# Performance work log

Hardware: AMD Instinct MI355X
Metric: run time of the kernel (lower is better)

Reference implementation:

```python
import jax, jax.numpy as jnp
import numpy as np

N = 50000        # total nodes across batch
K = 16           # max neighbors per node (padded with index 0)
E = 800000       # directed edges / messages
B = 1024         # molecules
MAXM = 48        # max nodes per molecule (padded with index 0)
FEATURE_FDIM = 9
ALL_FDIM = 10    # feature_dist_graph (9) + reshaped rij distance (1)
H = 64           # hidden_dim
NUM_ITERS = 2
NEG_INF = -1e9


def setup_inputs() -> dict:
    key = jax.random.key(0)
    ks = jax.random.split(key, 16)
    s = 1.0 / np.sqrt(H)
    return {
        "target_features": jax.random.normal(ks[0], (N, FEATURE_FDIM), jnp.float32),
        "feature_dist_graph": jax.random.normal(ks[1], (E, ALL_FDIM - 1), jnp.float32),
        "rij_dist_pairs": jax.random.uniform(ks[2], (E,), jnp.float32),
        "start_end_env": jax.random.randint(ks[3], (N, K), 0, N + 1),
        "b_scope": jax.random.randint(ks[4], (N, K), 0, E),
        "l_scope": jax.random.randint(ks[5], (B, MAXM), 0, N + 1),
        "scope_update": jax.random.randint(ks[6], (E,), 0, N + 1),
        "scope_update_lig": jax.random.randint(ks[7], (E,), 0, N + 1),
        "W_emb": jax.random.uniform(ks[8], (FEATURE_FDIM, H), jnp.float32, 0.1, 0.9),
        "b_emb": jnp.zeros((H,), jnp.float32),
        "W_dist": jax.random.uniform(ks[9], (ALL_FDIM, H), jnp.float32, 0.1, 0.9),
        "b_dist": jnp.zeros((H,), jnp.float32),
        "W_gat": jax.random.normal(ks[10], (H, H), jnp.float32) * s,
        "Wm_gat": jax.random.normal(ks[11], (H, H), jnp.float32) * s,
        "a_gat": jax.random.normal(ks[12], (2 * H,), jnp.float32) * s,
    }


def reference(target_features, feature_dist_graph, rij_dist_pairs,
              start_end_env, b_scope, l_scope, scope_update, scope_update_lig,
              W_emb, b_emb, W_dist, b_dist, W_gat, Wm_gat, a_gat):
    # node embedding over origin features
    h = target_features @ W_emb + b_emb                        # [N, H]
    # edge message embedding over pair features + distance
    msg_in = jnp.concatenate([feature_dist_graph, rij_dist_pairs[:, None]], axis=1)
    message = msg_in @ W_dist + b_dist                         # [E, H]
    # prepend zero pad row (index 0 = padding for ragged gathers)
    hp = jnp.concatenate([jnp.zeros((1, H), h.dtype), h], axis=0)  # [N+1, H]
    pad_mask = (start_end_env == 0)                            # [N, K]
    upd_mask = (scope_update_lig > 0).astype(h.dtype)[:, None]  # [E, 1]
    for _ in range(NUM_ITERS):
        nb = hp[start_end_env]                                 # [N, K, H] gather neighbors
        mg = message[b_scope]                                  # [N, K, H] gather messages
        Wn = nb @ W_gat                                        # [N, K, H]
        Wm = mg @ Wm_gat                                       # [N, K, H]
        # GAT attention logits: leaky_relu(a^T [Wn || Wm])
        logits = jax.nn.leaky_relu(
            jnp.einsum('nkh,h->nk', Wn, a_gat[:H]) +
            jnp.einsum('nkh,h->nk', Wm, a_gat[H:]), 0.2)       # [N, K]
        logits = jnp.where(pad_mask, NEG_INF, logits)
        alpha = jax.nn.softmax(logits, axis=1)                 # [N, K]
        new_h = jax.nn.elu(jnp.einsum('nk,nkh->nh', alpha, Wn + Wm))  # [N, H]
        hp = jnp.concatenate([jnp.zeros((1, H), new_h.dtype), new_h], axis=0)
        # scatter updated node features back into edge messages
        message = hp[scope_update] * upd_mask                  # [E, H]
    cmp_enc = hp[l_scope]                                      # [B, MAXM, H]
    return cmp_enc.sum(axis=1)                                 # [B, H]
```

## Files before the change

kernel.cpp:

```cpp
#include <hip/hip_runtime.h>
#include <hip/hip_bf16.h>

#define N_NODES 50000
#define K_NB 16
#define E_EDGES 800000
#define B_MOL 1024
#define MAXM_M 48
#define FDIM 9
#define ADIM 10
#define H 64
#define NEG_INF_F (-1e9f)
#define PRE_NODE_BLOCKS 196
#define EDGE_BLOCKS 3125

typedef __bf16 bf16x8 __attribute__((ext_vector_type(8)));
typedef float f32x4 __attribute__((ext_vector_type(4)));

__device__ inline float readlane_f(float v, int l) {
    return __int_as_float(__builtin_amdgcn_readlane(__float_as_int(v), l));
}
__device__ inline int readlane_i(int v, int l) {
    return __builtin_amdgcn_readlane(v, l);
}
__device__ inline float bf2f(unsigned u) {
    return __uint_as_float(u << 16);
}
__device__ inline unsigned short f2bf(float f) {
    unsigned x = __float_as_uint(f);
    return (unsigned short)((x + 0x7fffu + ((x >> 16) & 1u)) >> 16);
}

#define GLOAD_U16(dst, voff, sbase) \
    asm volatile("global_load_ushort %0, %1, %2" : "=v"(dst) : "v"(voff), "s"(sbase))
#define GLOAD_F32(dst, voff, sbase) \
    asm volatile("global_load_dword %0, %1, %2" : "=v"(dst) : "v"(voff), "s"(sbase))
#define GLOAD_DW(dst, voff, sbase) \
    asm volatile("global_load_dword %0, %1, %2" : "=v"(dst) : "v"(voff), "s"(sbase))

#define DRAIN16(a) \
    asm volatile("s_waitcnt vmcnt(0)" \
        : "+v"(a[0]), "+v"(a[1]), "+v"(a[2]), "+v"(a[3]), \
          "+v"(a[4]), "+v"(a[5]), "+v"(a[6]), "+v"(a[7]), \
          "+v"(a[8]), "+v"(a[9]), "+v"(a[10]), "+v"(a[11]), \
          "+v"(a[12]), "+v"(a[13]), "+v"(a[14]), "+v"(a[15]))
#define HOLD16(a) \
    asm volatile("" \
        : "+v"(a[0]), "+v"(a[1]), "+v"(a[2]), "+v"(a[3]), \
          "+v"(a[4]), "+v"(a[5]), "+v"(a[6]), "+v"(a[7]), \
          "+v"(a[8]), "+v"(a[9]), "+v"(a[10]), "+v"(a[11]), \
          "+v"(a[12]), "+v"(a[13]), "+v"(a[14]), "+v"(a[15]))

__global__ __launch_bounds__(256) void k_fold(
    const float* __restrict__ W_emb, const float* __restrict__ b_emb,
    const float* __restrict__ W_dist, const float* __restrict__ b_dist,
    const float* __restrict__ W_gat, const float* __restrict__ Wm_gat,
    const float* __restrict__ a_gat,
    float* __restrict__ W2, float* __restrict__ c2,
    float* __restrict__ W3, float* __restrict__ c3,
    float* __restrict__ wa, float* __restrict__ ca,
    float* __restrict__ va, float* __restrict__ vb,
    float* __restrict__ wv9, float* __restrict__ cv,
    unsigned short* __restrict__ WintT)
{
    __shared__ float s_va[64], s_vb[64];
    int tid = threadIdx.x;
    int h = tid & 63, g = tid >> 6;
    if (g == 0) {
        float acc = 0.f;
        for (int t = 0; t < H; ++t) acc += W_gat[h * H + t] * a_gat[t];
        s_va[h] = acc; va[h] = acc;
    } else if (g == 1) {
        float acc = 0.f;
        for (int t = 0; t < H; ++t) acc += Wm_gat[h * H + t] * a_gat[H + t];
        s_vb[h] = acc; vb[h] = acc;
    } else if (g == 2) {
        float acc = 0.f;
        for (int t = 0; t < H; ++t) acc += b_dist[t] * Wm_gat[t * H + h];
        c2[h] = acc;
    } else {
        float acc = 0.f;
        for (int t = 0; t < H; ++t) acc += b_emb[t] * W_gat[t * H + h];
        c3[h] = acc;
    }
    __syncthreads();
    for (int q = tid; q < 640; q += 256) {
        int j = q >> 6, hh = q & 63;
        float acc = 0.f;
        for (int t = 0; t < H; ++t) acc += W_dist[j * H + t] * Wm_gat[t * H + hh];
        W2[q] = acc;
    }
    for (int q = tid; q < 576; q += 256) {
        int j = q >> 6, hh = q & 63;
        float acc = 0.f;
        for (int t = 0; t < H; ++t) acc += W_emb[j * H + t] * W_gat[t * H + hh];
        W3[q] = acc;
    }
    for (int q = tid; q < H * 2 * H; q += 256) {
        int n = q >> 7, k = q & 127;
        float v = (k & 1) ? Wm_gat[(k >> 1) * H + n] : W_gat[(k >> 1) * H + n];
        WintT[q] = f2bf(v);
    }
    if (tid < ADIM) {
        float acc = 0.f;
        for (int t = 0; t < H; ++t) acc += W_dist[tid * H + t] * s_vb[t];
        wa[tid] = acc;
    } else if (tid == ADIM) {
        float acc = 0.f;
        for (int t = 0; t < H; ++t) acc += b_dist[t] * s_vb[t];
        ca[0] = acc;
    } else if (tid >= 16 && tid < 16 + FDIM) {
        int j = tid - 16;
        float acc = 0.f;
        for (int t = 0; t < H; ++t) acc += W_emb[j * H + t] * s_va[t];
        wv9[j] = acc;
    } else if (tid == 31) {
        float acc = 0.f;
        for (int t = 0; t < H; ++t) acc += b_emb[t] * s_va[t];
        cv[0] = acc;
    }
}

__global__ __launch_bounds__(256) void k_pre(
    const float* __restrict__ tf, const float* __restrict__ fdg,
    const float* __restrict__ rij,
    const int* __restrict__ su, const int* __restrict__ sul,
    const float* __restrict__ wa, const float* __restrict__ ca,
    const float* __restrict__ wv9, const float* __restrict__ cv,
    float* __restrict__ t1A, unsigned short* __restrict__ tfp,
    unsigned short* __restrict__ emsg, int* __restrict__ sue)
{
    int bid = blockIdx.x;
    if (bid < PRE_NODE_BLOCKS) {
        int n = bid * 256 + threadIdx.x;
        if (n == 0) {
            t1A[0] = 0.f;
            uint4 z = make_uint4(0, 0, 0, 0);
            ((uint4*)tfp)[0] = z; ((uint4*)tfp)[1] = z;
        }
        if (n >= N_NODES) return;
        float f[FDIM];
        float acc = cv[0];
#pragma unroll
        for (int j = 0; j < FDIM; ++j) {
            f[j] = tf[n * FDIM + j];
            acc += f[j] * wv9[j];
        }
        t1A[n + 1] = acc;
        unsigned rec[8];
#pragma unroll
        for (int j = 0; j < 4; ++j)
            rec[j] = (unsigned)f2bf(f[2 * j]) | ((unsigned)f2bf(f[2 * j + 1]) << 16);
        rec[4] = (unsigned)f2bf(f[8]);
        rec[5] = 0; rec[6] = 0; rec[7] = 0;
        uint4* dst = (uint4*)(tfp + (size_t)(n + 1) * 16);
        dst[0] = make_uint4(rec[0], rec[1], rec[2], rec[3]);
        dst[1] = make_uint4(rec[4], rec[5], rec[6], rec[7]);
    } else {
        int e = (bid - PRE_NODE_BLOCKS) * 256 + threadIdx.x;
        float f[ADIM];
#pragma unroll
        for (int j = 0; j < FDIM; ++j) f[j] = fdg[(size_t)e * FDIM + j];
        f[FDIM] = rij[e];
        float acc = ca[0];
#pragma unroll
        for (int j = 0; j < ADIM; ++j) acc += f[j] * wa[j];
        unsigned rec[8];
#pragma unroll
        for (int j = 0; j < 5; ++j)
            rec[j] = (unsigned)f2bf(f[2 * j]) | ((unsigned)f2bf(f[2 * j + 1]) << 16);
        rec[5] = __float_as_uint(acc);
        rec[6] = 0; rec[7] = 0;
        uint4* dst = (uint4*)(emsg + (size_t)e * 16);
        dst[0] = make_uint4(rec[0], rec[1], rec[2], rec[3]);
        dst[1] = make_uint4(rec[4], rec[5], rec[6], rec[7]);
        sue[e] = (sul[e] > 0) ? su[e] : 0;
    }
}

__global__ __launch_bounds__(256) void k_gat1(
    const int* __restrict__ sse, const int* __restrict__ bsc,
    const float* __restrict__ t1A, const unsigned short* __restrict__ tfp,
    const unsigned short* __restrict__ emsg,
    const float* __restrict__ W2, const float* __restrict__ c2,
    const float* __restrict__ W3, const float* __restrict__ c3,
    const float* __restrict__ va, const float* __restrict__ vb,
    unsigned short* __restrict__ hp2bf, float* __restrict__ t1B,
    float* __restrict__ t2B)
{
    int wave = threadIdx.x >> 6;
    int lane = threadIdx.x & 63;
    int n = blockIdx.x * 4 + wave;
    if (n == 0) {
        hp2bf[lane] = 0;
        if (lane == 0) { t1B[0] = 0.f; t2B[0] = 0.f; }
    }
    if (n >= N_NODES) return;

    int kidx = 0, ke = 0;
    float lg = NEG_INF_F;
    if (lane < K_NB) {
        kidx = sse[n * K_NB + lane];
        ke   = bsc[n * K_NB + lane];
        float g2 = __uint_as_float(*(const unsigned*)(emsg + (size_t)ke * 16 + 10));
        float p = t1A[kidx] + g2;
        p = (p > 0.f) ? p : 0.2f * p;
        lg = (kidx == 0) ? NEG_INF_F : p;
    }

    unsigned wn_u[K_NB], wm_u[K_NB];
    int offr = (lane & 15) * 2;
#pragma unroll
    for (int k = 0; k < K_NB; ++k) {
        const unsigned short* pk = tfp + (size_t)readlane_i(kidx, k) * 16;
        GLOAD_U16(wn_u[k], offr, pk);
    }
#pragma unroll
    for (int k = 0; k < K_NB; ++k) {
        const unsigned short* pe = emsg + (size_t)readlane_i(ke, k) * 16;
        GLOAD_U16(wm_u[k], offr, pe);
    }

    float m = lg;
#pragma unroll
    for (int o = 8; o > 0; o >>= 1) m = fmaxf(m, __shfl_xor(m, o, 64));
    float ex = __expf(lg - m);
    float s = ex;
#pragma unroll
    for (int o = 8; o > 0; o >>= 1) s += __shfl_xor(s, o, 64);
    float alpha = ex / s;

    DRAIN16(wn_u);
    HOLD16(wm_u);

    float fr = 0.f, frm = 0.f, beta = 0.f;
#pragma unroll
    for (int k = 0; k < K_NB; ++k) {
        float ak = readlane_f(alpha, k);
        fr  += ak * bf2f(wn_u[k]);
        frm += ak * bf2f(wm_u[k]);
        beta += (readlane_i(kidx, k) > 0) ? ak : 0.f;
    }
    float acc = c2[lane] + beta * c3[lane];
#pragma unroll
    for (int j = 0; j < FDIM; ++j) acc += readlane_f(fr, j) * W3[j * H + lane];
#pragma unroll
    for (int j = 0; j < ADIM; ++j) acc += readlane_f(frm, j) * W2[j * H + lane];
    float o = (acc > 0.f) ? acc : expm1f(acc);
    hp2bf[(size_t)(n + 1) * H + lane] = f2bf(o);
    float ta = o * va[lane], tb = o * vb[lane];
#pragma unroll
    for (int q = 32; q > 0; q >>= 1) {
        ta += __shfl_xor(ta, q, 64);
        tb += __shfl_xor(tb, q, 64);
    }
    if (lane == 0) { t1B[n + 1] = ta; t2B[n + 1] = tb; }
}

__global__ __launch_bounds__(1024) void k_gat2(
    const int* __restrict__ sse, const int* __restrict__ bsc,
    const int* __restrict__ sue,
    const float* __restrict__ t1B, const float* __restrict__ t2B,
    const unsigned short* __restrict__ hp2bf,
    const unsigned short* __restrict__ WintT,
    float* __restrict__ hp3)
{
    __shared__ unsigned s_rows[16][72];
    int wave = threadIdx.x >> 6;
    int lane = threadIdx.x & 63;
    int row  = blockIdx.x * 16 + wave;
    int n    = row - 1;

    float gn0 = 0.f, gn1 = 0.f, gm0 = 0.f, gm1 = 0.f;
    if (n >= 0 && n < N_NODES) {
        int kidx = 0, ksu = 0;
        float lg = NEG_INF_F;
        if (lane < K_NB) {
            kidx = sse[n * K_NB + lane];
            int ke = bsc[n * K_NB + lane];
            ksu = sue[ke];
            float p = t1B[kidx] + t2B[ksu];
            p = (p > 0.f) ? p : 0.2f * p;
            lg = (kidx == 0) ? NEG_INF_F : p;
        }

        int halfsel = lane >> 5;
        int cbyte = (lane & 31) * 4;
        unsigned wp[16];
#pragma unroll
        for (int g = 0; g < 8; ++g) {
            int rA = readlane_i(kidx, g);
            int rB = readlane_i(kidx, g + 8);
            int r  = halfsel ? rB : rA;
            GLOAD_DW(wp[g], r * 128 + cbyte, hp2bf);
        }
#pragma unroll
        for (int g = 0; g < 8; ++g) {
            int sA = readlane_i(ksu, g);
            int sB = readlane_i(ksu, g + 8);
            int rs = halfsel ? sB : sA;
            GLOAD_DW(wp[8 + g], rs * 128 + cbyte, hp2bf);
        }

        float m = lg;
#pragma unroll
        for (int o = 8; o > 0; o >>= 1) m = fmaxf(m, __shfl_xor(m, o, 64));
        float ex = __expf(lg - m);
        float s = ex;
#pragma unroll
        for (int o = 8; o > 0; o >>= 1) s += __shfl_xor(s, o, 64);
        float alpha = ex / s;

        DRAIN16(wp);

#pragma unroll
        for (int g = 0; g < 8; ++g) {
            float aA = readlane_f(alpha, g);
            float aB = readlane_f(alpha, g + 8);
            float av = halfsel ? aB : aA;
            unsigned wn = wp[g], wm = wp[8 + g];
            gn0 += av * bf2f(wn & 0xffffu);
            gn1 += av * bf2f(wn >> 16);
            gm0 += av * bf2f(wm & 0xffffu);
            gm1 += av * bf2f(wm >> 16);
        }
        gn0 += __shfl_xor(gn0, 32, 64);
        gn1 += __shfl_xor(gn1, 32, 64);
        gm0 += __shfl_xor(gm0, 32, 64);
        gm1 += __shfl_xor(gm1, 32, 64);
    }
    if (lane < 32) {
        s_rows[wave][2 * lane]     = (unsigned)f2bf(gn0) | ((unsigned)f2bf(gm0) << 16);
        s_rows[wave][2 * lane + 1] = (unsigned)f2bf(gn1) | ((unsigned)f2bf(gm1) << 16);
    }
    __syncthreads();

    if (wave < 4) {
        int t = wave;
        int m = lane & 15, q = lane >> 4;
        union UB { uint4 u; bf16x8 v; };
        bf16x8 bfr[4];
        const unsigned short* bp = WintT + (size_t)(t * 16 + m) * 128 + q * 8;
#pragma unroll
        for (int kk = 0; kk < 4; ++kk) {
            UB ub; ub.u = *(const uint4*)(bp + kk * 32);
            bfr[kk] = ub.v;
        }
        f32x4 acc = (f32x4){0.f, 0.f, 0.f, 0.f};
#pragma unroll
        for (int kk = 0; kk < 4; ++kk) {
            UB ua; ua.u = *(const uint4*)&s_rows[m][kk * 16 + q * 4];
            acc = __builtin_amdgcn_mfma_f32_16x16x32_bf16(ua.v, bfr[kk], acc, 0, 0, 0);
        }
        int row0 = blockIdx.x * 16;
#pragma unroll
        for (int r = 0; r < 4; ++r) {
            int rr = row0 + q * 4 + r;
            if (rr <= N_NODES) {
                float v = acc[r];
                hp3[(size_t)rr * H + t * 16 + m] = (v > 0.f) ? v : expm1f(v);
            }
        }
    }
}

__global__ __launch_bounds__(256) void k_out(
    const int* __restrict__ l_scope, const float* __restrict__ hp,
    float* __restrict__ out)
{
    int wave = threadIdx.x >> 6;
    int lane = threadIdx.x & 63;
    int b = blockIdx.x * 4 + wave;
    if (b >= B_MOL) return;
    int idx48 = (lane < MAXM_M) ? l_scope[b * MAXM_M + lane] : 0;
    float v[MAXM_M];
    int off = lane * 4;
#pragma unroll
    for (int m = 0; m < MAXM_M; ++m) {
        const float* pm = hp + (size_t)readlane_i(idx48, m) * H;
        GLOAD_F32(v[m], off, pm);
    }
    asm volatile("s_waitcnt vmcnt(0)"
        : "+v"(v[0]), "+v"(v[1]), "+v"(v[2]), "+v"(v[3]),
          "+v"(v[4]), "+v"(v[5]), "+v"(v[6]), "+v"(v[7]),
          "+v"(v[8]), "+v"(v[9]), "+v"(v[10]), "+v"(v[11]),
          "+v"(v[12]), "+v"(v[13]), "+v"(v[14]), "+v"(v[15]));
    asm volatile(""
        : "+v"(v[16]), "+v"(v[17]), "+v"(v[18]), "+v"(v[19]),
          "+v"(v[20]), "+v"(v[21]), "+v"(v[22]), "+v"(v[23]),
          "+v"(v[24]), "+v"(v[25]), "+v"(v[26]), "+v"(v[27]),
          "+v"(v[28]), "+v"(v[29]), "+v"(v[30]), "+v"(v[31]));
    asm volatile(""
        : "+v"(v[32]), "+v"(v[33]), "+v"(v[34]), "+v"(v[35]),
          "+v"(v[36]), "+v"(v[37]), "+v"(v[38]), "+v"(v[39]),
          "+v"(v[40]), "+v"(v[41]), "+v"(v[42]), "+v"(v[43]),
          "+v"(v[44]), "+v"(v[45]), "+v"(v[46]), "+v"(v[47]));
    float acc = 0.f;
#pragma unroll
    for (int m = 0; m < MAXM_M; ++m) acc += v[m];
    out[b * H + lane] = acc;
}

extern "C" void kernel_launch(void* const* d_in, const int* in_sizes, int n_in,
                              void* d_out, int out_size, void* d_ws, size_t ws_size,
                              hipStream_t stream)
{
    const float* tf     = (const float*)d_in[0];
    const float* fdg    = (const float*)d_in[1];
    const float* rij    = (const float*)d_in[2];
    const int*   sse    = (const int*)d_in[3];
    const int*   bsc    = (const int*)d_in[4];
    const int*   lsc    = (const int*)d_in[5];
    const int*   su     = (const int*)d_in[6];
    const int*   sul    = (const int*)d_in[7];
    const float* W_emb  = (const float*)d_in[8];
    const float* b_emb  = (const float*)d_in[9];
    const float* W_dist = (const float*)d_in[10];
    const float* b_dist = (const float*)d_in[11];
    const float* W_gat  = (const float*)d_in[12];
    const float* Wm_gat = (const float*)d_in[13];
    const float* a_gat  = (const float*)d_in[14];
    float* out = (float*)d_out;

    char* base = (char*)d_ws;
    size_t off = 0;
    auto alloc = [&](size_t bytes) {
        char* p = base + off;
        off = (off + bytes + 255) & ~(size_t)255;
        return p;
    };
    float* W2   = (float*)alloc(640 * 4);
    float* c2   = (float*)alloc(64 * 4);
    float* W3   = (float*)alloc(640 * 4);
    float* c3   = (float*)alloc(64 * 4);
    float* wa   = (float*)alloc(16 * 4);
    float* ca   = (float*)alloc(16 * 4);
    float* va   = (float*)alloc(64 * 4);
    float* vb   = (float*)alloc(64 * 4);
    float* wv9  = (float*)alloc(16 * 4);
    float* cv   = (float*)alloc(16 * 4);
    unsigned short* WintT = (unsigned short*)alloc(64 * 128 * 2);
    float* t1A  = (float*)alloc((size_t)(N_NODES + 1) * 4);
    float* t1B  = (float*)alloc((size_t)(N_NODES + 1) * 4);
    float* t2B  = (float*)alloc((size_t)(N_NODES + 1) * 4);
    int*   sue  = (int*)alloc((size_t)E_EDGES * 4);
    unsigned short* tfp   = (unsigned short*)alloc((size_t)(N_NODES + 1) * 16 * 2);
    unsigned short* hp2bf = (unsigned short*)alloc((size_t)(N_NODES + 1) * H * 2);
    char* big = alloc((size_t)E_EDGES * 32);
    unsigned short* emsg = (unsigned short*)big;
    float* hp3 = (float*)big;

    k_fold<<<dim3(1), dim3(256), 0, stream>>>(
        W_emb, b_emb, W_dist, b_dist, W_gat, Wm_gat, a_gat,
        W2, c2, W3, c3, wa, ca, va, vb, wv9, cv, WintT);

    k_pre<<<dim3(PRE_NODE_BLOCKS + EDGE_BLOCKS), dim3(256), 0, stream>>>(
        tf, fdg, rij, su, sul, wa, ca, wv9, cv, t1A, tfp, emsg, sue);

    k_gat1<<<dim3((N_NODES + 3) / 4), dim3(256), 0, stream>>>(
        sse, bsc, t1A, tfp, emsg, W2, c2, W3, c3, va, vb, hp2bf, t1B, t2B);

    k_gat2<<<dim3((N_NODES + 16) / 16), dim3(1024), 0, stream>>>(
        sse, bsc, sue, t1B, t2B, hp2bf, WintT, hp3);

    k_out<<<dim3(B_MOL / 4), dim3(256), 0, stream>>>(lsc, hp3, out);
}
```

Baseline: 208.2 us.

## Pack gat1 neighbor gathers across lane quarters and halve gat2 block size

In k_gat1, each of the four 16-lane quarters now gathers a different neighbor row, so 4 loads per array replace 16, with lane-partial sums combined by xor shuffles. Beta becomes a wave reduction instead of a serial readlane loop. k_gat2 moves to 512-thread blocks covering 8 rows, zero-pads the unused half of the shared MFMA tile, and only stores the valid rows. This cuts VGPR pressure and load-issue count in gat1 and raises block count in gat2, at the cost of extra shuffles and MFMA work wasted on padding rows.

```diff
diff --git a/kernel.cpp b/kernel.cpp
--- a/kernel.cpp
+++ b/kernel.cpp
@@ -43,12 +43,10 @@
           "+v"(a[4]), "+v"(a[5]), "+v"(a[6]), "+v"(a[7]), \
           "+v"(a[8]), "+v"(a[9]), "+v"(a[10]), "+v"(a[11]), \
           "+v"(a[12]), "+v"(a[13]), "+v"(a[14]), "+v"(a[15]))
-#define HOLD16(a) \
-    asm volatile("" \
+#define DRAIN8(a, b) \
+    asm volatile("s_waitcnt vmcnt(0)" \
         : "+v"(a[0]), "+v"(a[1]), "+v"(a[2]), "+v"(a[3]), \
-          "+v"(a[4]), "+v"(a[5]), "+v"(a[6]), "+v"(a[7]), \
-          "+v"(a[8]), "+v"(a[9]), "+v"(a[10]), "+v"(a[11]), \
-          "+v"(a[12]), "+v"(a[13]), "+v"(a[14]), "+v"(a[15]))
+          "+v"(b[0]), "+v"(b[1]), "+v"(b[2]), "+v"(b[3]))
 
 __global__ __launch_bounds__(256) void k_fold(
     const float* __restrict__ W_emb, const float* __restrict__ b_emb,
@@ -207,17 +205,31 @@
         lg = (kidx == 0) ? NEG_INF_F : p;
     }
 
-    unsigned wn_u[K_NB], wm_u[K_NB];
-    int offr = (lane & 15) * 2;
-#pragma unroll
-    for (int k = 0; k < K_NB; ++k) {
-        const unsigned short* pk = tfp + (size_t)readlane_i(kidx, k) * 16;
-        GLOAD_U16(wn_u[k], offr, pk);
-    }
-#pragma unroll
-    for (int k = 0; k < K_NB; ++k) {
-        const unsigned short* pe = emsg + (size_t)readlane_i(ke, k) * 16;
-        GLOAD_U16(wm_u[k], offr, pe);
+    int q1 = lane & 16;
+    int q2 = lane & 32;
+    int elem2 = (lane & 15) * 2;
+    unsigned wn_u[4], wm_u[4];
+#pragma unroll
+    for (int g = 0; g < 4; ++g) {
+        int rA = readlane_i(kidx, g);
+        int rB = readlane_i(kidx, g + 4);
+        int rC = readlane_i(kidx, g + 8);
+        int rD = readlane_i(kidx, g + 12);
+        int rLo = q1 ? rB : rA;
+        int rHi = q1 ? rD : rC;
+        int r   = q2 ? rHi : rLo;
+        GLOAD_U16(wn_u[g], r * 32 + elem2, tfp);
+    }
+#pragma unroll
+    for (int g = 0; g < 4; ++g) {
+        int rA = readlane_i(ke, g);
+        int rB = readlane_i(ke, g + 4);
+        int rC = readlane_i(ke, g + 8);
+        int rD = readlane_i(ke, g + 12);
+        int rLo = q1 ? rB : rA;
+        int rHi = q1 ? rD : rC;
+        int r   = q2 ? rHi : rLo;
+        GLOAD_U16(wm_u[g], r * 32 + elem2, emsg);
     }
 
     float m = lg;
@@ -229,17 +241,28 @@
     for (int o = 8; o > 0; o >>= 1) s += __shfl_xor(s, o, 64);
     float alpha = ex / s;
 
-    DRAIN16(wn_u);
-    HOLD16(wm_u);
-
-    float fr = 0.f, frm = 0.f, beta = 0.f;
-#pragma unroll
-    for (int k = 0; k < K_NB; ++k) {
-        float ak = readlane_f(alpha, k);
-        fr  += ak * bf2f(wn_u[k]);
-        frm += ak * bf2f(wm_u[k]);
-        beta += (readlane_i(kidx, k) > 0) ? ak : 0.f;
-    }
+    float beta = (kidx > 0) ? alpha : 0.f;
+#pragma unroll
+    for (int o = 1; o <= 32; o <<= 1) beta += __shfl_xor(beta, o, 64);
+
+    DRAIN8(wn_u, wm_u);
+
+    float fr = 0.f, frm = 0.f;
+#pragma unroll
+    for (int g = 0; g < 4; ++g) {
+        float aA = readlane_f(alpha, g);
+        float aB = readlane_f(alpha, g + 4);
+        float aC = readlane_f(alpha, g + 8);
+        float aD = readlane_f(alpha, g + 12);
+        float aLo = q1 ? aB : aA;
+        float aHi = q1 ? aD : aC;
+        float av  = q2 ? aHi : aLo;
+        fr  += av * bf2f(wn_u[g]);
+        frm += av * bf2f(wm_u[g]);
+    }
+    fr  += __shfl_xor(fr, 16, 64);  fr  += __shfl_xor(fr, 32, 64);
+    frm += __shfl_xor(frm, 16, 64); frm += __shfl_xor(frm, 32, 64);
+
     float acc = c2[lane] + beta * c3[lane];
 #pragma unroll
     for (int j = 0; j < FDIM; ++j) acc += readlane_f(fr, j) * W3[j * H + lane];
@@ -256,7 +279,7 @@
     if (lane == 0) { t1B[n + 1] = ta; t2B[n + 1] = tb; }
 }
 
-__global__ __launch_bounds__(1024) void k_gat2(
+__global__ __launch_bounds__(512) void k_gat2(
     const int* __restrict__ sse, const int* __restrict__ bsc,
     const int* __restrict__ sue,
     const float* __restrict__ t1B, const float* __restrict__ t2B,
@@ -267,8 +290,13 @@
     __shared__ unsigned s_rows[16][72];
     int wave = threadIdx.x >> 6;
     int lane = threadIdx.x & 63;
-    int row  = blockIdx.x * 16 + wave;
+    int row  = blockIdx.x * 8 + wave;
     int n    = row - 1;
+
+    if (lane < 32) {
+        s_rows[wave + 8][2 * lane]     = 0u;
+        s_rows[wave + 8][2 * lane + 1] = 0u;
+    }
 
     float gn0 = 0.f, gn1 = 0.f, gm0 = 0.f, gm1 = 0.f;
     if (n >= 0 && n < N_NODES) {
@@ -351,13 +379,15 @@
             UB ua; ua.u = *(const uint4*)&s_rows[m][kk * 16 + q * 4];
             acc = __builtin_amdgcn_mfma_f32_16x16x32_bf16(ua.v, bfr[kk], acc, 0, 0, 0);
         }
-        int row0 = blockIdx.x * 16;
-#pragma unroll
-        for (int r = 0; r < 4; ++r) {
-            int rr = row0 + q * 4 + r;
-            if (rr <= N_NODES) {
-                float v = acc[r];
-                hp3[(size_t)rr * H + t * 16 + m] = (v > 0.f) ? v : expm1f(v);
+        int row0 = blockIdx.x * 8;
+        if (q < 2) {
+#pragma unroll
+            for (int r = 0; r < 4; ++r) {
+                int rr = row0 + q * 4 + r;
+                if (rr <= N_NODES) {
+                    float v = acc[r];
+                    hp3[(size_t)rr * H + t * 16 + m] = (v > 0.f) ? v : expm1f(v);
+                }
             }
         }
     }
@@ -459,7 +489,7 @@
     k_gat1<<<dim3((N_NODES + 3) / 4), dim3(256), 0, stream>>>(
         sse, bsc, t1A, tfp, emsg, W2, c2, W3, c3, va, vb, hp2bf, t1B, t2B);
 
-    k_gat2<<<dim3((N_NODES + 16) / 16), dim3(1024), 0, stream>>>(
+    k_gat2<<<dim3((N_NODES + 8) / 8), dim3(512), 0, stream>>>(
         sse, bsc, sue, t1B, t2B, hp2bf, WintT, hp3);
 
     k_out<<<dim3(B_MOL / 4), dim3(256), 0, stream>>>(lsc, hp3, out);
```

Measured after the change: 202.8 us, median of 2. -2.6%, faster.

## Vectorize gat1 neighbor gathers with dwordx2 loads and shrink gat2 blocks

Applied to the files above, without the earlier changes.

In k_gat1, the 32 serialized per-neighbor ushort gathers are replaced by one dwordx2 gather per lane for node features and one for edge messages. Each group of four lanes covers one neighbor row, with indices broadcast via ds_bpermute, and the weighted sums are reduced with cross-lane shuffles. The separate edge logit load is also folded into the message gather. k_gat2 moves from 1024-thread blocks of 16 rows to 512-thread blocks of 8 rows, zero-padding the unused MFMA rows, which costs half of the MFMA work but gives smaller blocks and finer scheduling.

```diff
diff --git a/kernel.cpp b/kernel.cpp
--- a/kernel.cpp
+++ b/kernel.cpp
@@ -15,6 +15,7 @@
 
 typedef __bf16 bf16x8 __attribute__((ext_vector_type(8)));
 typedef float f32x4 __attribute__((ext_vector_type(4)));
+typedef unsigned u32x2 __attribute__((ext_vector_type(2)));
 
 __device__ inline float readlane_f(float v, int l) {
     return __int_as_float(__builtin_amdgcn_readlane(__float_as_int(v), l));
@@ -36,15 +37,11 @@
     asm volatile("global_load_dword %0, %1, %2" : "=v"(dst) : "v"(voff), "s"(sbase))
 #define GLOAD_DW(dst, voff, sbase) \
     asm volatile("global_load_dword %0, %1, %2" : "=v"(dst) : "v"(voff), "s"(sbase))
+#define GLOAD_X2(dst, voff, sbase) \
+    asm volatile("global_load_dwordx2 %0, %1, %2" : "=v"(dst) : "v"(voff), "s"(sbase))
 
 #define DRAIN16(a) \
     asm volatile("s_waitcnt vmcnt(0)" \
-        : "+v"(a[0]), "+v"(a[1]), "+v"(a[2]), "+v"(a[3]), \
-          "+v"(a[4]), "+v"(a[5]), "+v"(a[6]), "+v"(a[7]), \
-          "+v"(a[8]), "+v"(a[9]), "+v"(a[10]), "+v"(a[11]), \
-          "+v"(a[12]), "+v"(a[13]), "+v"(a[14]), "+v"(a[15]))
-#define HOLD16(a) \
-    asm volatile("" \
         : "+v"(a[0]), "+v"(a[1]), "+v"(a[2]), "+v"(a[3]), \
           "+v"(a[4]), "+v"(a[5]), "+v"(a[6]), "+v"(a[7]), \
           "+v"(a[8]), "+v"(a[9]), "+v"(a[10]), "+v"(a[11]), \
@@ -197,29 +194,32 @@
     if (n >= N_NODES) return;
 
     int kidx = 0, ke = 0;
-    float lg = NEG_INF_F;
     if (lane < K_NB) {
         kidx = sse[n * K_NB + lane];
         ke   = bsc[n * K_NB + lane];
-        float g2 = __uint_as_float(*(const unsigned*)(emsg + (size_t)ke * 16 + 10));
-        float p = t1A[kidx] + g2;
+    }
+
+    int srcaddr = (lane >> 2) * 4;
+    int rk = __builtin_amdgcn_ds_bpermute(srcaddr, kidx);
+    int re = __builtin_amdgcn_ds_bpermute(srcaddr, ke);
+    int j8 = (lane & 3) * 8;
+
+    u32x2 wn2, wm2;
+    GLOAD_X2(wn2, rk * 32 + j8, tfp);
+    GLOAD_X2(wm2, re * 32 + j8, emsg);
+    float t1v = t1A[kidx];
+
+    asm volatile("s_waitcnt vmcnt(0)" : "+v"(wn2), "+v"(wm2), "+v"(t1v));
+
+    float g2 = __int_as_float(
+        __builtin_amdgcn_ds_bpermute(lane * 16 + 8, (int)wm2.y));
+
+    float lg = NEG_INF_F;
+    if (lane < K_NB) {
+        float p = t1v + g2;
         p = (p > 0.f) ? p : 0.2f * p;
         lg = (kidx == 0) ? NEG_INF_F : p;
     }
-
-    unsigned wn_u[K_NB], wm_u[K_NB];
-    int offr = (lane & 15) * 2;
-#pragma unroll
-    for (int k = 0; k < K_NB; ++k) {
-        const unsigned short* pk = tfp + (size_t)readlane_i(kidx, k) * 16;
-        GLOAD_U16(wn_u[k], offr, pk);
-    }
-#pragma unroll
-    for (int k = 0; k < K_NB; ++k) {
-        const unsigned short* pe = emsg + (size_t)readlane_i(ke, k) * 16;
-        GLOAD_U16(wm_u[k], offr, pe);
-    }
-
     float m = lg;
 #pragma unroll
     for (int o = 8; o > 0; o >>= 1) m = fmaxf(m, __shfl_xor(m, o, 64));
@@ -229,22 +229,45 @@
     for (int o = 8; o > 0; o >>= 1) s += __shfl_xor(s, o, 64);
     float alpha = ex / s;
 
-    DRAIN16(wn_u);
-    HOLD16(wm_u);
-
-    float fr = 0.f, frm = 0.f, beta = 0.f;
-#pragma unroll
-    for (int k = 0; k < K_NB; ++k) {
-        float ak = readlane_f(alpha, k);
-        fr  += ak * bf2f(wn_u[k]);
-        frm += ak * bf2f(wm_u[k]);
-        beta += (readlane_i(kidx, k) > 0) ? ak : 0.f;
-    }
+    float beta = (kidx > 0) ? alpha : 0.f;
+#pragma unroll
+    for (int o = 1; o <= 32; o <<= 1) beta += __shfl_xor(beta, o, 64);
+
+    float av = __int_as_float(
+        __builtin_amdgcn_ds_bpermute(srcaddr, __float_as_int(alpha)));
+
+    unsigned nlo = wn2.x, nhi = wn2.y;
+    unsigned mlo = wm2.x;
+    unsigned mhi = ((lane & 3) == 2) ? 0u : wm2.y;
+    float fr0 = av * bf2f(nlo & 0xffffu);
+    float fr1 = av * bf2f(nlo >> 16);
+    float fr2 = av * bf2f(nhi & 0xffffu);
+    float fr3 = av * bf2f(nhi >> 16);
+    float fm0 = av * bf2f(mlo & 0xffffu);
+    float fm1 = av * bf2f(mlo >> 16);
+    float fm2 = av * bf2f(mhi & 0xffffu);
+    float fm3 = av * bf2f(mhi >> 16);
+#pragma unroll
+    for (int o = 4; o <= 32; o <<= 1) {
+        fr0 += __shfl_xor(fr0, o, 64); fr1 += __shfl_xor(fr1, o, 64);
+        fr2 += __shfl_xor(fr2, o, 64); fr3 += __shfl_xor(fr3, o, 64);
+        fm0 += __shfl_xor(fm0, o, 64); fm1 += __shfl_xor(fm1, o, 64);
+        fm2 += __shfl_xor(fm2, o, 64); fm3 += __shfl_xor(fm3, o, 64);
+    }
+
     float acc = c2[lane] + beta * c3[lane];
 #pragma unroll
-    for (int j = 0; j < FDIM; ++j) acc += readlane_f(fr, j) * W3[j * H + lane];
-#pragma unroll
-    for (int j = 0; j < ADIM; ++j) acc += readlane_f(frm, j) * W2[j * H + lane];
+    for (int e = 0; e < FDIM; ++e) {
+        float v = ((e & 3) == 0) ? fr0 : ((e & 3) == 1) ? fr1
+                : ((e & 3) == 2) ? fr2 : fr3;
+        acc += readlane_f(v, e >> 2) * W3[e * H + lane];
+    }
+#pragma unroll
+    for (int e = 0; e < ADIM; ++e) {
+        float v = ((e & 3) == 0) ? fm0 : ((e & 3) == 1) ? fm1
+                : ((e & 3) == 2) ? fm2 : fm3;
+        acc += readlane_f(v, e >> 2) * W2[e * H + lane];
+    }
     float o = (acc > 0.f) ? acc : expm1f(acc);
     hp2bf[(size_t)(n + 1) * H + lane] = f2bf(o);
     float ta = o * va[lane], tb = o * vb[lane];
@@ -256,7 +279,7 @@
     if (lane == 0) { t1B[n + 1] = ta; t2B[n + 1] = tb; }
 }
 
-__global__ __launch_bounds__(1024) void k_gat2(
+__global__ __launch_bounds__(512) void k_gat2(
     const int* __restrict__ sse, const int* __restrict__ bsc,
     const int* __restrict__ sue,
     const float* __restrict__ t1B, const float* __restrict__ t2B,
@@ -267,8 +290,13 @@
     __shared__ unsigned s_rows[16][72];
     int wave = threadIdx.x >> 6;
     int lane = threadIdx.x & 63;
-    int row  = blockIdx.x * 16 + wave;
+    int row  = blockIdx.x * 8 + wave;
     int n    = row - 1;
+
+    if (lane < 32) {
+        s_rows[wave + 8][2 * lane]     = 0u;
+        s_rows[wave + 8][2 * lane + 1] = 0u;
+    }
 
     float gn0 = 0.f, gn1 = 0.f, gm0 = 0.f, gm1 = 0.f;
     if (n >= 0 && n < N_NODES) {
@@ -351,13 +379,15 @@
             UB ua; ua.u = *(const uint4*)&s_rows[m][kk * 16 + q * 4];
             acc = __builtin_amdgcn_mfma_f32_16x16x32_bf16(ua.v, bfr[kk], acc, 0, 0, 0);
         }
-        int row0 = blockIdx.x * 16;
-#pragma unroll
-        for (int r = 0; r < 4; ++r) {
-            int rr = row0 + q * 4 + r;
-            if (rr <= N_NODES) {
-                float v = acc[r];
-                hp3[(size_t)rr * H + t * 16 + m] = (v > 0.f) ? v : expm1f(v);
+        int row0 = blockIdx.x * 8;
+        if (q < 2) {
+#pragma unroll
+            for (int r = 0; r < 4; ++r) {
+                int rr = row0 + q * 4 + r;
+                if (rr <= N_NODES) {
+                    float v = acc[r];
+                    hp3[(size_t)rr * H + t * 16 + m] = (v > 0.f) ? v : expm1f(v);
+                }
             }
         }
     }
@@ -459,7 +489,7 @@
     k_gat1<<<dim3((N_NODES + 3) / 4), dim3(256), 0, stream>>>(
         sse, bsc, t1A, tfp, emsg, W2, c2, W3, c3, va, vb, hp2bf, t1B, t2B);
 
-    k_gat2<<<dim3((N_NODES + 16) / 16), dim3(1024), 0, stream>>>(
+    k_gat2<<<dim3((N_NODES + 8) / 8), dim3(512), 0, stream>>>(
         sse, bsc, sue, t1B, t2B, hp2bf, WintT, hp3);
 
     k_out<<<dim3(B_MOL / 4), dim3(256), 0, stream>>>(lsc, hp3, out);
```

Measured after the change: 209.1 us. Within noise of the previous version (+0.4%).
